# Kernel tuning notes

Hardware: AMD Instinct MI355X
Metric: run time of the kernel (lower is better)

The kernel has to match this reference:

```python
import jax, jax.numpy as jnp
import numpy as np

B, T, C = 2, 2048, 4096
NH, NKV, HD = 32, 8, 128
GROUPS = NH // NKV
THETA = 10000.0


def _rope_tables(seq_len, dim, theta, dtype):
    inv_freq = 1.0 / (theta ** (jnp.arange(0, dim, 2, dtype=jnp.float32) / dim))
    t = jnp.arange(seq_len, dtype=jnp.float32)
    freqs = jnp.outer(t, inv_freq)            # [T, dim/2]
    emb = jnp.concatenate([freqs, freqs], -1)  # [T, dim]
    return jnp.cos(emb).astype(dtype), jnp.sin(emb).astype(dtype)


def _rotate_half(x):
    h = x.shape[-1] // 2
    return jnp.concatenate([-x[..., h:], x[..., :h]], axis=-1)


def setup_inputs() -> dict:
    key = jax.random.key(0)
    ks = jax.random.split(key, 5)
    s = 1.0 / np.sqrt(C)
    return {
        "x": jax.random.normal(ks[0], (B, T, C), jnp.float32),
        "wq": jax.random.normal(ks[1], (C, NH * HD), jnp.float32) * s,
        "wk": jax.random.normal(ks[2], (C, NKV * HD), jnp.float32) * s,
        "wv": jax.random.normal(ks[3], (C, NKV * HD), jnp.float32) * s,
        "wo": jax.random.normal(ks[4], (NH * HD, C), jnp.float32) * s,
    }


def reference(x, wq, wk, wv, wo):
    b, t, c = x.shape
    q = (x @ wq).reshape(b, t, NH, HD).transpose(0, 2, 1, 3)    # [B,NH,T,HD]
    k = (x @ wk).reshape(b, t, NKV, HD).transpose(0, 2, 1, 3)   # [B,NKV,T,HD]
    v = (x @ wv).reshape(b, t, NKV, HD).transpose(0, 2, 1, 3)
    cos, sin = _rope_tables(t, HD, THETA, x.dtype)              # [T,HD]
    cos = cos[None, None]
    sin = sin[None, None]
    q = q * cos + _rotate_half(q) * sin
    k = k * cos + _rotate_half(k) * sin
    # GQA: broadcast KV heads over groups via einsum instead of materializing repeat
    qg = q.reshape(b, NKV, GROUPS, t, HD)
    scores = jnp.einsum('bkgqd,bkld->bkgql', qg, k) * (HD ** -0.5)  # [B,NKV,G,T,T]
    causal = jnp.triu(jnp.full((t, t), -jnp.inf, dtype=x.dtype), k=1)
    scores = scores + causal
    attn = jax.nn.softmax(scores, axis=-1)
    out = jnp.einsum('bkgql,bkld->bkgqd', attn, v)              # [B,NKV,G,T,HD]
    out = out.reshape(b, NH, t, HD).transpose(0, 2, 1, 3).reshape(b, t, NH * HD)
    return out @ wo
```

## Files before the change

### kernel.cpp

```cpp
#include <hip/hip_runtime.h>
#include <hip/hip_bf16.h>
#include <math.h>

#define B_ 2
#define T_ 2048
#define C_ 4096
#define NH_ 32
#define NKV_ 8
#define HD_ 128
#define M_ (B_*T_)
#define QKVN_ (NH_*HD_ + 2*NKV_*HD_)

using bf16 = __hip_bfloat16;
typedef __bf16 bf16x8 __attribute__((ext_vector_type(8)));
typedef float f32x4 __attribute__((ext_vector_type(4)));

__device__ inline f32x4 mfma16(bf16x8 a, bf16x8 b, f32x4 c) {
    return __builtin_amdgcn_mfma_f32_16x16x32_bf16(a, b, c, 0, 0, 0);
}

__global__ __launch_bounds__(256) void cast_f32_bf16(const float* __restrict__ in,
                                                     bf16* __restrict__ out, int n4) {
    int i = blockIdx.x * 256 + threadIdx.x;
    if (i >= n4) return;
    float4 v = reinterpret_cast<const float4*>(in)[i];
    union { bf16 h[4]; uint2 u; } o;
    o.h[0] = __float2bfloat16(v.x);
    o.h[1] = __float2bfloat16(v.y);
    o.h[2] = __float2bfloat16(v.z);
    o.h[3] = __float2bfloat16(v.w);
    reinterpret_cast<uint2*>(out)[i] = o.u;
}

__global__ __launch_bounds__(256) void transpose_cast(const float* __restrict__ in,
                                                      bf16* __restrict__ out, int K, int N) {
    __shared__ float tile[32][33];
    int tx = threadIdx.x & 31, ty = threadIdx.x >> 5;
    int n0 = blockIdx.x << 5, k0 = blockIdx.y << 5;
#pragma unroll
    for (int p = 0; p < 4; ++p)
        tile[p*8 + ty][tx] = in[(size_t)(k0 + p*8 + ty) * N + n0 + tx];
    __syncthreads();
#pragma unroll
    for (int p = 0; p < 4; ++p)
        out[(size_t)(n0 + p*8 + ty) * K + k0 + tx] = __float2bfloat16(tile[tx][p*8 + ty]);
}

__global__ __launch_bounds__(256) void rope_tab(float2* __restrict__ tab) {
    int idx = blockIdx.x * 256 + threadIdx.x;
    int i = idx & 63, t = idx >> 6;
    float inv = exp2f((float)i * -0.20762050593045952f);
    float th = (float)t * inv;
    tab[idx] = make_float2(cosf(th), sinf(th));
}

#define GEMM_PROLOG_AND_LOOP(LDB_ROW_EXPR)                                              \
    f32x4 acc[8][4] = {};                                                               \
    bf16x8 a[4][2], b0[2][2], b1[2][2];                                                 \
    STAGE_HALF(Ag, 0,     0, 0, 0); STAGE_HALF(Ag, 0,     0, 0, 1);                     \
    STAGE_HALF(Bg, 65536, 0, 0, 0); STAGE_HALF(Bg, 65536, 0, 0, 1);                     \
    STAGE_HALF(Bg, 65536, 1, 1, 0); STAGE_HALF(Bg, 65536, 1, 1, 1);                     \
    asm volatile("s_waitcnt vmcnt(4)" ::: "memory");                                    \
    BAR();                                                                              \
    for (int it = 0; it < (nt >> 1); ++it) {                                            \
        const int u = 2 * it;                                                           \
        const bool more = (u + 2) < nt;                                                 \
        READ_A(0, 0); READ_B(0, 0, b0);                                                 \
        STAGE_HALF(Ag, 0, u + 1, 1, 0);                                                 \
        MFMA_Q(0, 0, b0);                                                               \
        BAR();                                                                          \
        READ_B(0, 1, b1);                                                               \
        STAGE_HALF(Ag, 0, u + 1, 1, 1);                                                 \
        MFMA_Q(0, 2, b1);                                                               \
        BAR();                                                                          \
        READ_A(0, 1);                                                                   \
        if (more) STAGE_HALF(Bg, 65536, u + 2, 0, 0);                                   \
        MFMA_Q(4, 2, b1);                                                               \
        BAR();                                                                          \
        if (more) STAGE_HALF(Bg, 65536, u + 2, 0, 1);                                   \
        MFMA_Q(4, 0, b0);                                                               \
        if (more) asm volatile("s_waitcnt vmcnt(8)" ::: "memory");                      \
        else      asm volatile("s_waitcnt vmcnt(4)" ::: "memory");                      \
        BAR();                                                                          \
        READ_A(1, 0); READ_B(1, 0, b0);                                                 \
        if (more) STAGE_HALF(Ag, 0, u + 2, 0, 0);                                       \
        MFMA_Q(0, 0, b0);                                                               \
        BAR();                                                                          \
        READ_B(1, 1, b1);                                                               \
        if (more) STAGE_HALF(Ag, 0, u + 2, 0, 1);                                       \
        MFMA_Q(0, 2, b1);                                                               \
        if (more) asm volatile("s_waitcnt vmcnt(8)" ::: "memory");                      \
        else      asm volatile("s_waitcnt vmcnt(0)" ::: "memory");                      \
        BAR();                                                                          \
        READ_A(1, 1);                                                                   \
        if (more) STAGE_HALF(Bg, 65536, u + 3, 1, 0);                                   \
        MFMA_Q(4, 2, b1);                                                               \
        BAR();                                                                          \
        if (more) STAGE_HALF(Bg, 65536, u + 3, 1, 1);                                   \
        MFMA_Q(4, 0, b0);                                                               \
        if (more) asm volatile("s_waitcnt vmcnt(4)" ::: "memory");                      \
        else      asm volatile("s_waitcnt vmcnt(0)" ::: "memory");                      \
        BAR();                                                                          \
    }

#define GEMM_COMMON_DEFS                                                                \
    __shared__ __align__(16) char lds[131072];                                          \
    const int tid = threadIdx.x;                                                        \
    const int wid = tid >> 6, lane = tid & 63;                                          \
    const int lq = lane & 15, lg = lane >> 4;                                           \
    const int wrow = wid >> 2, wcol = wid & 3;                                          \
    const int nwg = gridDim.x;                                                          \
    const int q8 = nwg >> 3;                                                            \
    const int wg = (blockIdx.x & 7) * q8 + (blockIdx.x >> 3);                           \
    const int nby = M >> 8;                                                             \
    const int by = wg % nby, bx = wg / nby;                                             \
    const int brow = by << 8, bcol = bx << 8;                                           \
    const bf16* Ag = A + (size_t)brow * K;                                              \
    const bf16* Bg = Bt + (size_t)bcol * K;                                             \
    const int nt = K >> 6;                                                              \
    const int srow = (wid << 3) + (lane >> 3);                                          \
    const int schunk = (lane & 7) ^ ((lane >> 3) & 7);

#define STAGE_HALF(gbase, ldsoff, t2, cbuf, hf)                                         \
    {                                                                                   \
        _Pragma("unroll")                                                               \
        for (int l = 0; l < 2; ++l) {                                                   \
            const int r0 = (hf) * 128 + l * 64;                                         \
            const char* src = (const char*)(gbase) +                                    \
                ((size_t)(r0 + srow) * K + (size_t)(t2) * 64) * 2 + schunk * 16;        \
            char* dst = &lds[(ldsoff) + (cbuf) * 32768 + (r0 + (wid << 3)) * 128];      \
            __builtin_amdgcn_global_load_lds(                                           \
                (const __attribute__((address_space(1))) void*)src,                     \
                (__attribute__((address_space(3))) void*)dst, 16, 0, 0);                \
        }                                                                               \
    }

#define LDA(cbuf, mh, mf, ks) \
    (*(const bf16x8*)&lds[(cbuf)*32768 + (wrow*128 + (mh)*64 + (mf)*16 + lq)*128 + ((((ks)*4 + lg)) ^ (lq & 7))*16])

#define READ_A(cbuf, mh) \
    { _Pragma("unroll") for (int mf = 0; mf < 4; ++mf) { a[mf][0] = LDA(cbuf, mh, mf, 0); a[mf][1] = LDA(cbuf, mh, mf, 1); } }
#define READ_B(cbuf, nh, breg) \
    { _Pragma("unroll") for (int nf = 0; nf < 2; ++nf) { breg[nf][0] = LDB(cbuf, nh, nf, 0); breg[nf][1] = LDB(cbuf, nh, nf, 1); } }
#define MFMA_Q(am, an, breg)                                                     \
    { __builtin_amdgcn_s_setprio(1);                                             \
      _Pragma("unroll") for (int mf = 0; mf < 4; ++mf)                           \
          _Pragma("unroll") for (int nf = 0; nf < 2; ++nf)                       \
              _Pragma("unroll") for (int ks = 0; ks < 2; ++ks)                   \
                  acc[(am) + mf][(an) + nf] = mfma16(a[mf][ks], breg[nf][ks],    \
                                                     acc[(am) + mf][(an) + nf]); \
      __builtin_amdgcn_s_setprio(0); }
#define BAR() __builtin_amdgcn_s_barrier()

__device__ inline void store_out(float* p, float v) { *p = v; }
__device__ inline void store_out(bf16*  p, float v) { *p = __float2bfloat16(v); }

template <typename OutT>
__global__ __launch_bounds__(512, 2) void gemm256(const bf16* __restrict__ A,
                                                  const bf16* __restrict__ Bt,
                                                  OutT* __restrict__ C,
                                                  int M, int N, int K) {
    GEMM_COMMON_DEFS
#define LDB(cbuf, nh, nf, ks) \
    (*(const bf16x8*)&lds[65536 + (cbuf)*32768 + (wcol*64 + (nh)*32 + (nf)*16 + lq)*128 + ((((ks)*4 + lg)) ^ (lq & 7))*16])
    GEMM_PROLOG_AND_LOOP(plain)
#undef LDB
#pragma unroll
    for (int mf = 0; mf < 8; ++mf)
#pragma unroll
        for (int nf = 0; nf < 4; ++nf)
#pragma unroll
            for (int r = 0; r < 4; ++r) {
                int row = brow + wrow * 128 + mf * 16 + lg * 4 + r;
                int col = bcol + wcol * 64 + nf * 16 + lq;
                store_out(&C[(size_t)row * N + col], acc[mf][nf][r]);
            }
}

__global__ __launch_bounds__(512, 2) void gemm_qkv(const bf16* __restrict__ A,
                                                   const bf16* __restrict__ Bt,
                                                   bf16* __restrict__ q_r,
                                                   bf16* __restrict__ k_r,
                                                   bf16* __restrict__ vbuf,
                                                   const float2* __restrict__ tab,
                                                   int M, int N, int K) {
    GEMM_COMMON_DEFS
#define LDB(cbuf, nh, nf, ks) \
    (*(const bf16x8*)&lds[65536 + (cbuf)*32768 + (((wcol>>1)*128 + (wcol&1)*32 + (nh)*64 + (nf)*16 + lq))*128 + ((((ks)*4 + lg)) ^ (lq & 7))*16])
    GEMM_PROLOG_AND_LOOP(remap)
#undef LDB

    const int trow = brow + wrow * 128;
    if (bcol >= 5120) {
#pragma unroll
        for (int mf = 0; mf < 8; ++mf)
#pragma unroll
            for (int j = 0; j < 4; ++j)
#pragma unroll
                for (int r = 0; r < 4; ++r) {
                    int row = trow + mf*16 + lg*4 + r;
                    int col = bcol + (wcol>>1)*128 + (wcol&1)*32 + (j>>1)*64 + (j&1)*16 + lq;
                    vbuf[(size_t)row * (NKV_*HD_) + (col - 5120)] = __float2bfloat16(acc[mf][j][r]);
                }
    } else {
        const bool isQ = (bcol < 4096);
        const float sc = isQ ? 0.12751741230963214f : 1.0f;
#pragma unroll
        for (int mf = 0; mf < 8; ++mf)
#pragma unroll
            for (int j = 0; j < 2; ++j)
#pragma unroll
                for (int r = 0; r < 4; ++r) {
                    int row = trow + mf*16 + lg*4 + r;
                    int bb = row >> 11, tt = row & 2047;
                    int i  = (wcol&1)*32 + j*16 + lq;
                    float2 cs = tab[tt*64 + i];
                    float x0 = acc[mf][j][r], x1 = acc[mf][j+2][r];
                    float y0 = (x0*cs.x - x1*cs.y) * sc;
                    float y1 = (x1*cs.x + x0*cs.y) * sc;
                    int col0 = bcol + (wcol>>1)*128 + i;
                    if (isQ) {
                        int h = col0 >> 7, hd = col0 & 127;
                        bf16* dst = q_r + ((size_t)(bb*NH_ + h)*T_ + tt)*HD_;
                        dst[hd]      = __float2bfloat16(y0);
                        dst[hd + 64] = __float2bfloat16(y1);
                    } else {
                        int ch = col0 - 4096;
                        int h = ch >> 7, hd = ch & 127;
                        bf16* dst = k_r + ((size_t)(bb*NKV_ + h)*T_ + tt)*HD_;
                        dst[hd]      = __float2bfloat16(y0);
                        dst[hd + 64] = __float2bfloat16(y1);
                    }
                }
    }
}

#undef GEMM_PROLOG_AND_LOOP
#undef GEMM_COMMON_DEFS
#undef STAGE_HALF
#undef LDA
#undef READ_A
#undef READ_B
#undef MFMA_Q
#undef BAR

__global__ __launch_bounds__(256) void vtrans(const bf16* __restrict__ vbuf,
                                              bf16* __restrict__ vt) {
    __shared__ bf16 tile[32][33];
    int gx = blockIdx.x;
    int dt = gx & 3;
    int tt = (gx >> 2) & 63;
    int kv = (gx >> 8) & 7;
    int b  = gx >> 11;
    int d0 = dt * 32, t0 = tt * 32;
    int tx = threadIdx.x & 31, ty = threadIdx.x >> 5;

    const bf16* src = vbuf + (size_t)(b * T_ + t0) * (NKV_*HD_) + kv * HD_ + d0;
#pragma unroll
    for (int p = 0; p < 4; ++p)
        tile[p*8 + ty][tx] = src[(size_t)(p*8 + ty) * (NKV_*HD_) + tx];
    __syncthreads();
    bf16* dst = vt + ((size_t)((b * NKV_ + kv) * HD_ + d0)) * T_ + t0;
#pragma unroll
    for (int p = 0; p < 4; ++p)
        dst[(size_t)(p*8 + ty) * T_ + tx] = tile[tx][p*8 + ty];
}

__global__ __launch_bounds__(1024) void fattn(const bf16* __restrict__ Q,
                                              const bf16* __restrict__ Kt,
                                              const bf16* __restrict__ VT,
                                              bf16* __restrict__ O) {
    const int lin = blockIdx.x;
    const int kv = lin & 7;
    const int b  = (lin >> 3) & 1;
    const int idx = lin >> 4;
    const int h  = kv * 4 + (idx & 3);
    const int jp = idx >> 2;

    const int tid = threadIdx.x, wid = tid >> 6, lane = tid & 63;
    const int lq = lane & 15, lg = lane >> 4;

    const bf16* Kp = Kt + (size_t)(b * NKV_ + kv) * T_ * HD_;
    const bf16* Vp = VT + (size_t)(b * NKV_ + kv) * HD_ * T_;

    __shared__ __align__(16) bf16 Ks[2][64][128];
    __shared__ __align__(16) bf16 Vs[2][128][64];
    __shared__ __align__(16) bf16 p_lds[16][16][72];

    const float THR_L2 = 11.5416f;

#define STAGE_KV(cbuf, tt)                                                           \
    { {                                                                              \
        int krow = wid * 4 + (lane >> 4);                                            \
        int kch  = (lane & 15) ^ (krow & 15);                                        \
        const bf16* ksrc = Kp + (size_t)((tt) * 64 + krow) * HD_ + kch * 8;          \
        __builtin_amdgcn_global_load_lds(                                            \
            (const __attribute__((address_space(1))) void*)ksrc,                     \
            (__attribute__((address_space(3))) void*)&Ks[cbuf][wid*4][0],            \
            16, 0, 0);                                                               \
      }                                                                              \
      {                                                                              \
        int vrow = wid * 8 + (lane >> 3);                                            \
        int vch  = (lane & 7) ^ (vrow & 7);                                          \
        const bf16* vsrc = Vp + (size_t)vrow * T_ + (tt) * 64 + vch * 8;             \
        __builtin_amdgcn_global_load_lds(                                            \
            (const __attribute__((address_space(1))) void*)vsrc,                     \
            (__attribute__((address_space(3))) void*)&Vs[cbuf][wid*8][0],            \
            16, 0, 0);                                                               \
      } }

    for (int half = 0; half < 2; ++half) {
        const int qt = half ? (7 - jp) : jp;
        const int q0 = qt * 256 + wid * 16;
        const int kv_end = q0 + 16;
        const int NT = qt * 4 + 4;

        const bf16* Qp = Q + ((size_t)(b * NH_ + h) * T_ + q0) * HD_;
        bf16x8 qf[4];
#pragma unroll
        for (int c = 0; c < 4; ++c)
            qf[c] = *(const bf16x8*)&Qp[(size_t)lq * HD_ + c * 32 + lg * 8];

        f32x4 oacc[8] = {};
        float m_r = -INFINITY;
        float l_r = 0.f;

        STAGE_KV(0, 0);
        STAGE_KV(1, 1);
        asm volatile("s_waitcnt vmcnt(2)" ::: "memory");
        __builtin_amdgcn_s_barrier();

        for (int t = 0; t < NT; ++t) {
            const int cb = t & 1;
            const int t0 = t * 64;

            if (t0 < kv_end) {
                f32x4 st[4] = {};
#pragma unroll
                for (int n = 0; n < 4; ++n) {
                    bf16x8 kf[4];
#pragma unroll
                    for (int c = 0; c < 4; ++c)
                        kf[c] = *(const bf16x8*)((const char*)&Ks[cb][n*16 + lq][0]
                                                  + (((c*4 + lg) ^ lq) << 4));
                    __builtin_amdgcn_s_setprio(1);
#pragma unroll
                    for (int c = 0; c < 4; ++c)
                        st[n] = mfma16(kf[c], qf[c], st[n]);
                    __builtin_amdgcn_s_setprio(0);
                }

                const int qq = q0 + lq;
#pragma unroll
                for (int n = 0; n < 4; ++n)
#pragma unroll
                    for (int r = 0; r < 4; ++r) {
                        int kk = t0 + n*16 + lg*4 + r;
                        if (kk > qq) st[n][r] = -INFINITY;
                    }

                float rmax = st[0][0];
#pragma unroll
                for (int n = 0; n < 4; ++n)
#pragma unroll
                    for (int r = 0; r < 4; ++r) rmax = fmaxf(rmax, st[n][r]);
                rmax = fmaxf(rmax, __shfl_xor(rmax, 16));
                rmax = fmaxf(rmax, __shfl_xor(rmax, 32));

                if (__any(rmax - m_r > THR_L2)) {
                    float mnew = fmaxf(m_r, rmax);
                    float alpha = exp2f(m_r - mnew);
                    m_r = mnew;
                    l_r *= alpha;
#pragma unroll
                    for (int r = 0; r < 4; ++r) {
                        float a_pv = __shfl(alpha, lg*4 + r);
#pragma unroll
                        for (int f = 0; f < 8; ++f) oacc[f][r] *= a_pv;
                    }
                }

                float rsum = 0.f;
#pragma unroll
                for (int n = 0; n < 4; ++n)
#pragma unroll
                    for (int r = 0; r < 4; ++r) {
                        float p = exp2f(st[n][r] - m_r);
                        st[n][r] = p;
                        rsum += p;
                    }
                rsum += __shfl_xor(rsum, 16);
                rsum += __shfl_xor(rsum, 32);
                l_r += rsum;

#pragma unroll
                for (int n = 0; n < 4; ++n) {
                    union { bf16 hh[4]; uint2 u; } pk;
#pragma unroll
                    for (int r = 0; r < 4; ++r) pk.hh[r] = __float2bfloat16(st[n][r]);
                    *(uint2*)&p_lds[wid][lq][n*16 + lg*4] = pk.u;
                }

#pragma unroll
                for (int ks = 0; ks < 2; ++ks) {
                    bf16x8 pa = *(const bf16x8*)&p_lds[wid][lq][ks*32 + lg*8];
                    bf16x8 vf[8];
#pragma unroll
                    for (int f = 0; f < 8; ++f)
                        vf[f] = *(const bf16x8*)((const char*)&Vs[cb][f*16 + lq][0]
                                                  + (((ks*4 + lg) ^ (lq & 7)) << 4));
                    __builtin_amdgcn_s_setprio(1);
#pragma unroll
                    for (int f = 0; f < 8; ++f)
                        oacc[f] = mfma16(pa, vf[f], oacc[f]);
                    __builtin_amdgcn_s_setprio(0);
                }
            }

            __builtin_amdgcn_s_barrier();
            if (t + 2 < NT) {
                STAGE_KV(cb, t + 2);
                asm volatile("s_waitcnt vmcnt(2)" ::: "memory");
            } else {
                asm volatile("s_waitcnt vmcnt(0)" ::: "memory");
            }
            __builtin_amdgcn_s_barrier();
        }

        {
            float rinv = __builtin_amdgcn_rcpf(l_r);
#pragma unroll
            for (int r = 0; r < 4; ++r) {
                float rl = __shfl(rinv, lg*4 + r);
                int row = q0 + lg*4 + r;
#pragma unroll
                for (int f = 0; f < 8; ++f) {
                    int d = f*16 + lq;
                    O[((size_t)(b * T_ + row) * NH_ + h) * HD_ + d] =
                        __float2bfloat16(oacc[f][r] * rl);
                }
            }
        }
    }
#undef STAGE_KV
}

extern "C" void kernel_launch(void* const* d_in, const int* in_sizes, int n_in,
                              void* d_out, int out_size, void* d_ws, size_t ws_size,
                              hipStream_t stream) {
    const float* x  = (const float*)d_in[0];
    const float* wq = (const float*)d_in[1];
    const float* wk = (const float*)d_in[2];
    const float* wv = (const float*)d_in[3];
    const float* wo = (const float*)d_in[4];
    float* out = (float*)d_out;

    bf16* ws    = (bf16*)d_ws;
    bf16* xb    = ws;
    bf16* wqkvT = xb + (size_t)M_ * C_;
    bf16* qr_wo = wqkvT + (size_t)QKVN_ * C_;
    bf16* region = qr_wo + (size_t)C_ * C_;
    bf16* k_r  = region;
    bf16* vt   = k_r + (size_t)B_ * NKV_ * T_ * HD_;
    bf16* vbuf = vt  + (size_t)B_ * NKV_ * T_ * HD_;
    float2* tab = (float2*)(vbuf + (size_t)B_ * T_ * NKV_ * HD_);

    bf16* attn = xb;

    cast_f32_bf16<<<(M_ * C_ / 4 + 255) / 256, 256, 0, stream>>>(x, xb, M_ * C_ / 4);
    transpose_cast<<<dim3(128, 128), 256, 0, stream>>>(wq, wqkvT, C_, NH_ * HD_);
    transpose_cast<<<dim3(32, 128), 256, 0, stream>>>(wk, wqkvT + (size_t)(NH_ * HD_) * C_, C_, NKV_ * HD_);
    transpose_cast<<<dim3(32, 128), 256, 0, stream>>>(wv, wqkvT + (size_t)(NH_ * HD_ + NKV_ * HD_) * C_, C_, NKV_ * HD_);
    rope_tab<<<(T_ * 64) / 256, 256, 0, stream>>>(tab);

    gemm_qkv<<<dim3((QKVN_ / 256) * (M_ / 256)), 512, 0, stream>>>(
        xb, wqkvT, qr_wo, k_r, vbuf, tab, M_, QKVN_, C_);

    vtrans<<<B_ * NKV_ * (T_ / 32) * (HD_ / 32), 256, 0, stream>>>(vbuf, vt);

    fattn<<<dim3(256), 1024, 0, stream>>>(qr_wo, k_r, vt, attn);

    transpose_cast<<<dim3(128, 128), 256, 0, stream>>>(wo, qr_wo, NH_ * HD_, C_);
    gemm256<float><<<dim3((C_ / 256) * (M_ / 256)), 512, 0, stream>>>(attn, qr_wo, out, M_, C_, C_);
}
```

Measured before the change: 502.0 us.

## Split fused QKV GEMM into a Q GEMM and a smaller-tile KV GEMM

The single QKV projection launch, with 256x256 tiles, is split into two launches. The Q projection keeps the 256x256 tile kernel with RoPE and scaling in its epilogue. A new KV kernel uses 128x256 tiles and 96KB of LDS and writes roped K and raw V. The aim is to give each launch a block count that matches the number of compute units, which reduces the tail-wave imbalance of the fused grid. The cost is an extra launch and a less efficient, smaller tile for K/V. The prefetch guard for the u+3 stage is also tightened.

New measurement: 478.1 us. 4.8% less time.

```diff
diff --git a/kernel.cpp b/kernel.cpp
--- a/kernel.cpp
+++ b/kernel.cpp
@@ -54,7 +54,7 @@
     tab[idx] = make_float2(cosf(th), sinf(th));
 }
 
-#define GEMM_PROLOG_AND_LOOP(LDB_ROW_EXPR)                                              \
+#define GEMM_PROLOG_AND_LOOP(TAG)                                                       \
     f32x4 acc[8][4] = {};                                                               \
     bf16x8 a[4][2], b0[2][2], b1[2][2];                                                 \
     STAGE_HALF(Ag, 0,     0, 0, 0); STAGE_HALF(Ag, 0,     0, 0, 1);                     \
@@ -65,6 +65,7 @@
     for (int it = 0; it < (nt >> 1); ++it) {                                            \
         const int u = 2 * it;                                                           \
         const bool more = (u + 2) < nt;                                                 \
+        const bool more3 = (u + 3) < nt;                                                \
         READ_A(0, 0); READ_B(0, 0, b0);                                                 \
         STAGE_HALF(Ag, 0, u + 1, 1, 0);                                                 \
         MFMA_Q(0, 0, b0);                                                               \
@@ -93,13 +94,13 @@
         else      asm volatile("s_waitcnt vmcnt(0)" ::: "memory");                      \
         BAR();                                                                          \
         READ_A(1, 1);                                                                   \
-        if (more) STAGE_HALF(Bg, 65536, u + 3, 1, 0);                                   \
+        if (more3) STAGE_HALF(Bg, 65536, u + 3, 1, 0);                                  \
         MFMA_Q(4, 2, b1);                                                               \
         BAR();                                                                          \
-        if (more) STAGE_HALF(Bg, 65536, u + 3, 1, 1);                                   \
+        if (more3) STAGE_HALF(Bg, 65536, u + 3, 1, 1);                                  \
         MFMA_Q(4, 0, b0);                                                               \
-        if (more) asm volatile("s_waitcnt vmcnt(4)" ::: "memory");                      \
-        else      asm volatile("s_waitcnt vmcnt(0)" ::: "memory");                      \
+        if (more3) asm volatile("s_waitcnt vmcnt(4)" ::: "memory");                     \
+        else       asm volatile("s_waitcnt vmcnt(0)" ::: "memory");                     \
         BAR();                                                                          \
     }
 
@@ -180,10 +181,8 @@
 __global__ __launch_bounds__(512, 2) void gemm_qkv(const bf16* __restrict__ A,
                                                    const bf16* __restrict__ Bt,
                                                    bf16* __restrict__ q_r,
-                                                   bf16* __restrict__ k_r,
-                                                   bf16* __restrict__ vbuf,
                                                    const float2* __restrict__ tab,
-                                                   int M, int N, int K) {
+                                                   int M, int K) {
     GEMM_COMMON_DEFS
 #define LDB(cbuf, nh, nf, ks) \
     (*(const bf16x8*)&lds[65536 + (cbuf)*32768 + (((wcol>>1)*128 + (wcol&1)*32 + (nh)*64 + (nf)*16 + lq))*128 + ((((ks)*4 + lg)) ^ (lq & 7))*16])
@@ -191,48 +190,26 @@
 #undef LDB
 
     const int trow = brow + wrow * 128;
-    if (bcol >= 5120) {
-#pragma unroll
-        for (int mf = 0; mf < 8; ++mf)
-#pragma unroll
-            for (int j = 0; j < 4; ++j)
-#pragma unroll
-                for (int r = 0; r < 4; ++r) {
-                    int row = trow + mf*16 + lg*4 + r;
-                    int col = bcol + (wcol>>1)*128 + (wcol&1)*32 + (j>>1)*64 + (j&1)*16 + lq;
-                    vbuf[(size_t)row * (NKV_*HD_) + (col - 5120)] = __float2bfloat16(acc[mf][j][r]);
-                }
-    } else {
-        const bool isQ = (bcol < 4096);
-        const float sc = isQ ? 0.12751741230963214f : 1.0f;
-#pragma unroll
-        for (int mf = 0; mf < 8; ++mf)
-#pragma unroll
-            for (int j = 0; j < 2; ++j)
-#pragma unroll
-                for (int r = 0; r < 4; ++r) {
-                    int row = trow + mf*16 + lg*4 + r;
-                    int bb = row >> 11, tt = row & 2047;
-                    int i  = (wcol&1)*32 + j*16 + lq;
-                    float2 cs = tab[tt*64 + i];
-                    float x0 = acc[mf][j][r], x1 = acc[mf][j+2][r];
-                    float y0 = (x0*cs.x - x1*cs.y) * sc;
-                    float y1 = (x1*cs.x + x0*cs.y) * sc;
-                    int col0 = bcol + (wcol>>1)*128 + i;
-                    if (isQ) {
-                        int h = col0 >> 7, hd = col0 & 127;
-                        bf16* dst = q_r + ((size_t)(bb*NH_ + h)*T_ + tt)*HD_;
-                        dst[hd]      = __float2bfloat16(y0);
-                        dst[hd + 64] = __float2bfloat16(y1);
-                    } else {
-                        int ch = col0 - 4096;
-                        int h = ch >> 7, hd = ch & 127;
-                        bf16* dst = k_r + ((size_t)(bb*NKV_ + h)*T_ + tt)*HD_;
-                        dst[hd]      = __float2bfloat16(y0);
-                        dst[hd + 64] = __float2bfloat16(y1);
-                    }
-                }
-    }
+    const float sc = 0.12751741230963214f;
+#pragma unroll
+    for (int mf = 0; mf < 8; ++mf)
+#pragma unroll
+        for (int j = 0; j < 2; ++j)
+#pragma unroll
+            for (int r = 0; r < 4; ++r) {
+                int row = trow + mf*16 + lg*4 + r;
+                int bb = row >> 11, tt = row & 2047;
+                int i  = (wcol&1)*32 + j*16 + lq;
+                float2 cs = tab[tt*64 + i];
+                float x0 = acc[mf][j][r], x1 = acc[mf][j+2][r];
+                float y0 = (x0*cs.x - x1*cs.y) * sc;
+                float y1 = (x1*cs.x + x0*cs.y) * sc;
+                int col0 = bcol + (wcol>>1)*128 + i;
+                int h = col0 >> 7, hd = col0 & 127;
+                bf16* dst = q_r + ((size_t)(bb*NH_ + h)*T_ + tt)*HD_;
+                dst[hd]      = __float2bfloat16(y0);
+                dst[hd + 64] = __float2bfloat16(y1);
+            }
 }
 
 #undef GEMM_PROLOG_AND_LOOP
@@ -243,6 +220,166 @@
 #undef READ_B
 #undef MFMA_Q
 #undef BAR
+
+__global__ __launch_bounds__(512, 2) void gemm_kv(const bf16* __restrict__ A,
+                                                  const bf16* __restrict__ BtKV,
+                                                  bf16* __restrict__ k_r,
+                                                  bf16* __restrict__ vbuf,
+                                                  const float2* __restrict__ tab,
+                                                  int M, int K) {
+    __shared__ __align__(16) char lds[98304];
+    const int tid = threadIdx.x;
+    const int wid = tid >> 6, lane = tid & 63;
+    const int lq = lane & 15, lg = lane >> 4;
+    const int wrow = wid >> 2, wcol = wid & 3;
+
+    const int nwg = gridDim.x;
+    const int q8 = nwg >> 3;
+    const int wg = (blockIdx.x & 7) * q8 + (blockIdx.x >> 3);
+    const int nby = M >> 7;
+    const int by = wg % nby, bx = wg / nby;
+    const int brow = by << 7;
+    const int bcolr = bx << 8;
+
+    const bf16* Ag = A + (size_t)brow * K;
+    const bf16* Bg = BtKV + (size_t)bcolr * K;
+    const int nt = K >> 6;
+
+    const int srow = (wid << 3) + (lane >> 3);
+    const int schunk = (lane & 7) ^ ((lane >> 3) & 7);
+
+#define KV_STAGE_A(t2, cbuf, hf)                                                        \
+    {                                                                                   \
+        const char* src = (const char*)Ag +                                             \
+            ((size_t)((hf) * 64 + srow) * K + (size_t)(t2) * 64) * 2 + schunk * 16;     \
+        char* dst = &lds[(cbuf) * 16384 + ((hf) * 64 + (wid << 3)) * 128];              \
+        __builtin_amdgcn_global_load_lds(                                               \
+            (const __attribute__((address_space(1))) void*)src,                         \
+            (__attribute__((address_space(3))) void*)dst, 16, 0, 0);                    \
+    }
+#define KV_STAGE_B(t2, cbuf, hf)                                                        \
+    {                                                                                   \
+        _Pragma("unroll")                                                               \
+        for (int l = 0; l < 2; ++l) {                                                   \
+            const int r0 = (hf) * 128 + l * 64;                                         \
+            const char* src = (const char*)Bg +                                         \
+                ((size_t)(r0 + srow) * K + (size_t)(t2) * 64) * 2 + schunk * 16;        \
+            char* dst = &lds[32768 + (cbuf) * 32768 + (r0 + (wid << 3)) * 128];         \
+            __builtin_amdgcn_global_load_lds(                                           \
+                (const __attribute__((address_space(1))) void*)src,                     \
+                (__attribute__((address_space(3))) void*)dst, 16, 0, 0);                \
+        }                                                                               \
+    }
+#define KV_LDA(cbuf, mh, f, ks) \
+    (*(const bf16x8*)&lds[(cbuf)*16384 + (wrow*64 + (mh)*32 + (f)*16 + lq)*128 + ((((ks)*4 + lg)) ^ (lq & 7))*16])
+#define KV_LDB(cbuf, nh, nf, ks) \
+    (*(const bf16x8*)&lds[32768 + (cbuf)*32768 + (((wcol>>1)*128 + (wcol&1)*32 + (nh)*64 + (nf)*16 + lq))*128 + ((((ks)*4 + lg)) ^ (lq & 7))*16])
+#define KV_READ_A(cbuf, mh) \
+    { _Pragma("unroll") for (int f = 0; f < 2; ++f) { a[f][0] = KV_LDA(cbuf, mh, f, 0); a[f][1] = KV_LDA(cbuf, mh, f, 1); } }
+#define KV_READ_B(cbuf, nh, breg) \
+    { _Pragma("unroll") for (int nf = 0; nf < 2; ++nf) { breg[nf][0] = KV_LDB(cbuf, nh, nf, 0); breg[nf][1] = KV_LDB(cbuf, nh, nf, 1); } }
+#define KV_MFMA(am, an, breg)                                                    \
+    { __builtin_amdgcn_s_setprio(1);                                             \
+      _Pragma("unroll") for (int f = 0; f < 2; ++f)                              \
+          _Pragma("unroll") for (int nf = 0; nf < 2; ++nf)                       \
+              _Pragma("unroll") for (int ks = 0; ks < 2; ++ks)                   \
+                  acc[(am) + f][(an) + nf] = mfma16(a[f][ks], breg[nf][ks],      \
+                                                    acc[(am) + f][(an) + nf]);   \
+      __builtin_amdgcn_s_setprio(0); }
+#define KV_BAR() __builtin_amdgcn_s_barrier()
+
+    f32x4 acc[4][4] = {};
+    bf16x8 a[2][2], b0[2][2], b1[2][2];
+
+    KV_STAGE_A(0, 0, 0); KV_STAGE_A(0, 0, 1);
+    KV_STAGE_B(0, 0, 0); KV_STAGE_B(0, 0, 1);
+    KV_STAGE_B(1, 1, 0); KV_STAGE_B(1, 1, 1);
+    asm volatile("s_waitcnt vmcnt(4)" ::: "memory");
+    KV_BAR();
+
+    for (int it = 0; it < (nt >> 1); ++it) {
+        const int u = 2 * it;
+        const bool more = (u + 2) < nt;
+        const bool more3 = (u + 3) < nt;
+
+        KV_READ_A(0, 0); KV_READ_B(0, 0, b0);
+        KV_STAGE_A(u + 1, 1, 0);
+        KV_MFMA(0, 0, b0);
+        KV_BAR();
+        KV_READ_B(0, 1, b1);
+        KV_STAGE_A(u + 1, 1, 1);
+        KV_MFMA(0, 2, b1);
+        KV_BAR();
+        KV_READ_A(0, 1);
+        if (more) KV_STAGE_B(u + 2, 0, 0);
+        KV_MFMA(2, 2, b1);
+        KV_BAR();
+        if (more) KV_STAGE_B(u + 2, 0, 1);
+        KV_MFMA(2, 0, b0);
+        if (more) asm volatile("s_waitcnt vmcnt(4)" ::: "memory");
+        else      asm volatile("s_waitcnt vmcnt(0)" ::: "memory");
+        KV_BAR();
+        KV_READ_A(1, 0); KV_READ_B(1, 0, b0);
+        if (more) KV_STAGE_A(u + 2, 0, 0);
+        KV_MFMA(0, 0, b0);
+        KV_BAR();
+        KV_READ_B(1, 1, b1);
+        if (more) KV_STAGE_A(u + 2, 0, 1);
+        KV_MFMA(0, 2, b1);
+        KV_BAR();
+        KV_READ_A(1, 1);
+        if (more3) KV_STAGE_B(u + 3, 1, 0);
+        KV_MFMA(2, 2, b1);
+        KV_BAR();
+        if (more3) KV_STAGE_B(u + 3, 1, 1);
+        KV_MFMA(2, 0, b0);
+        if (more3) asm volatile("s_waitcnt vmcnt(4)" ::: "memory");
+        else       asm volatile("s_waitcnt vmcnt(0)" ::: "memory");
+        KV_BAR();
+    }
+
+    const int trow = brow + wrow * 64;
+    if (bcolr >= 1024) {
+#pragma unroll
+        for (int mf = 0; mf < 4; ++mf)
+#pragma unroll
+            for (int j = 0; j < 4; ++j)
+#pragma unroll
+                for (int r = 0; r < 4; ++r) {
+                    int row = trow + (mf>>1)*32 + (mf&1)*16 + lg*4 + r;
+                    int col = bcolr + (wcol>>1)*128 + (wcol&1)*32 + (j>>1)*64 + (j&1)*16 + lq - 1024;
+                    vbuf[(size_t)row * (NKV_*HD_) + col] = __float2bfloat16(acc[mf][j][r]);
+                }
+    } else {
+#pragma unroll
+        for (int mf = 0; mf < 4; ++mf)
+#pragma unroll
+            for (int j = 0; j < 2; ++j)
+#pragma unroll
+                for (int r = 0; r < 4; ++r) {
+                    int row = trow + (mf>>1)*32 + (mf&1)*16 + lg*4 + r;
+                    int bb = row >> 11, tt = row & 2047;
+                    int i  = (wcol&1)*32 + j*16 + lq;
+                    float2 cs = tab[tt*64 + i];
+                    float x0 = acc[mf][j][r], x1 = acc[mf][j+2][r];
+                    float y0 = x0*cs.x - x1*cs.y;
+                    float y1 = x1*cs.x + x0*cs.y;
+                    int col0 = bcolr + (wcol>>1)*128 + i;
+                    int h = col0 >> 7, hd = col0 & 127;
+                    bf16* dst = k_r + ((size_t)(bb*NKV_ + h)*T_ + tt)*HD_;
+                    dst[hd]      = __float2bfloat16(y0);
+                    dst[hd + 64] = __float2bfloat16(y1);
+                }
+    }
+#undef KV_STAGE_A
+#undef KV_STAGE_B
+#undef KV_LDA
+#undef KV_LDB
+#undef KV_READ_A
+#undef KV_READ_B
+#undef KV_MFMA
+#undef KV_BAR
+}
 
 __global__ __launch_bounds__(256) void vtrans(const bf16* __restrict__ vbuf,
                                               bf16* __restrict__ vt) {
@@ -473,8 +610,10 @@
     transpose_cast<<<dim3(32, 128), 256, 0, stream>>>(wv, wqkvT + (size_t)(NH_ * HD_ + NKV_ * HD_) * C_, C_, NKV_ * HD_);
     rope_tab<<<(T_ * 64) / 256, 256, 0, stream>>>(tab);
 
-    gemm_qkv<<<dim3((QKVN_ / 256) * (M_ / 256)), 512, 0, stream>>>(
-        xb, wqkvT, qr_wo, k_r, vbuf, tab, M_, QKVN_, C_);
+    gemm_qkv<<<dim3((C_ / 256) * (M_ / 256)), 512, 0, stream>>>(
+        xb, wqkvT, qr_wo, tab, M_, C_);
+    gemm_kv<<<dim3(256), 512, 0, stream>>>(
+        xb, wqkvT + (size_t)(NH_ * HD_) * C_, k_r, vbuf, tab, M_, C_);
 
     vtrans<<<B_ * NKV_ * (T_ / 32) * (HD_ / 32), 256, 0, stream>>>(vbuf, vt);
 
```
